# Optimization experiments

Measured on AMD Instinct MI355X. Metric: run time of the kernel, lower is better.

## Reference

```python
import jax, jax.numpy as jnp
import numpy as np
from jax import lax

B, C, H, W = 16, 128, 128, 128
C8, C16 = C // 8, C // 16
LN_EPS = 1e-5


def dct_mat(N):
    # torch_dct.dct (norm=None): X_k = 2 * sum_n x_n cos(pi*(2n+1)k/(2N))
    n = jnp.arange(N, dtype=jnp.float32)
    k = jnp.arange(N, dtype=jnp.float32)
    return 2.0 * jnp.cos(jnp.pi * (2.0 * n[None, :] + 1.0) * k[:, None] / (2.0 * N))


def setup_inputs() -> dict:
    key = jax.random.key(0)
    ks = jax.random.split(key, 20)
    s = 0.05
    return {
        "x": jax.random.normal(ks[0], (B, C, H, W), dtype=jnp.float32),
        # channel attention (1x1 convs acting on GAP -> stored as dense [out,in])
        "ca_w1": jax.random.normal(ks[1], (C8, C), dtype=jnp.float32) * s,
        "ca_b1": jnp.zeros((C8,), jnp.float32),
        "ca_w2": jax.random.normal(ks[2], (C, C8), dtype=jnp.float32) * s,
        "ca_b2": jnp.zeros((C,), jnp.float32),
        # spatial attention 9x9 conv -> 1 channel
        "sa_w": jax.random.normal(ks[3], (1, C, 9, 9), dtype=jnp.float32) * s,
        "sa_b": jnp.zeros((1,), jnp.float32),
        # frequency channel attention MLP
        "fa_w1": jax.random.normal(ks[4], (C8, C), dtype=jnp.float32) * s,
        "fa_b1": jnp.zeros((C8,), jnp.float32),
        "fa_w2": jax.random.normal(ks[5], (C, C8), dtype=jnp.float32) * s,
        "fa_b2": jnp.zeros((C,), jnp.float32),
        # global context block
        "gc_mask_w": jax.random.normal(ks[6], (C,), dtype=jnp.float32) * s,
        "gc_mask_b": jnp.zeros((), jnp.float32),
        "gc_t1_w": jax.random.normal(ks[7], (C16, C), dtype=jnp.float32) * s,
        "gc_t1_b": jnp.zeros((C16,), jnp.float32),
        "gc_ln_g": jnp.ones((C16,), jnp.float32),
        "gc_ln_b": jnp.zeros((C16,), jnp.float32),
        "gc_t2_w": jax.random.normal(ks[8], (C, C16), dtype=jnp.float32) * s,
        "gc_t2_b": jnp.zeros((C,), jnp.float32),
        # branch mixing weights + output 1x1 conv
        "alpha": jnp.ones((4,), jnp.float32),
        "out_w": jax.random.normal(ks[9], (C, C), dtype=jnp.float32) * s,
        "out_b": jnp.zeros((C,), jnp.float32),
    }


def reference(x, ca_w1, ca_b1, ca_w2, ca_b2, sa_w, sa_b,
              fa_w1, fa_b1, fa_w2, fa_b2,
              gc_mask_w, gc_mask_b, gc_t1_w, gc_t1_b, gc_ln_g, gc_ln_b,
              gc_t2_w, gc_t2_b, alpha, out_w, out_b):
    b, c, h, w = x.shape
    # --- channel attention (SE-style) ---
    gap = x.mean(axis=(2, 3))                                   # [B,C]
    hca = jax.nn.relu(gap @ ca_w1.T + ca_b1)
    ca = jax.nn.sigmoid(hca @ ca_w2.T + ca_b2)                  # [B,C]
    ac = x * ca[:, :, None, None]
    # --- spatial attention (9x9 conv -> sigmoid gate) ---
    smap = lax.conv_general_dilated(x, sa_w, (1, 1), ((4, 4), (4, 4)),
                                    dimension_numbers=("NCHW", "OIHW", "NCHW"))
    as_ = jax.nn.sigmoid(smap + sa_b[None, :, None, None]) * x
    # --- frequency channel attention (DCT-II 2d, mean over freq) ---
    Dw = dct_mat(w)
    Dh = dct_mat(h)
    xf = jnp.einsum("bchw,kw->bchk", x, Dw)
    xf = jnp.einsum("bchk,lh->bclk", xf, Dh)                    # [B,C,H,W] freq
    favg = xf.mean(axis=(2, 3))                                 # [B,C]
    hfa = jax.nn.relu(favg @ fa_w1.T + fa_b1)
    fwt = jax.nn.sigmoid(hfa @ fa_w2.T + fa_b2)
    af = x * fwt[:, :, None, None]
    # --- global context block ---
    mask = jnp.einsum("bchw,c->bhw", x, gc_mask_w) + gc_mask_b  # [B,H,W]
    mask = jax.nn.softmax(mask.reshape(b, h * w), axis=-1)      # [B,HW]
    ctx = jnp.einsum("bcp,bp->bc", x.reshape(b, c, h * w), mask)  # [B,C]
    t = ctx @ gc_t1_w.T + gc_t1_b                               # [B,C/16]
    mu = t.mean(axis=-1, keepdims=True)
    var = ((t - mu) ** 2).mean(axis=-1, keepdims=True)
    t = (t - mu) * lax.rsqrt(var + LN_EPS) * gc_ln_g + gc_ln_b
    t = jax.nn.relu(t)
    ctx2 = t @ gc_t2_w.T + gc_t2_b                              # [B,C]
    ag = x + ctx2[:, :, None, None]
    # --- softmax-weighted fusion + output 1x1 conv ---
    wts = jax.nn.softmax(alpha)
    fused = wts[0] * ac + wts[1] * as_ + wts[2] * af + wts[3] * ag
    return jnp.einsum("bchw,oc->bohw", fused, out_w) + out_b[None, :, None, None]
```

## Files before the change

kernel.cpp:

```cpp
#include <hip/hip_runtime.h>
#include <math.h>

#define B_   16
#define C_   128
#define W_   128
#define HW_  16384

#define OFF_SARR 0
#define OFF_GAP  128
#define OFF_FAVG 2176
#define OFF_CTX  4224
#define OFF_G    6272
#define OFF_CB   8320
#define OFF_WTS  10368
#define OFF_PMAX 10496
#define OFF_PSUM 10752
#define OFF_SMX  11008
#define OFF_SINV 11024
#define OFF_M    16384
#define OFF_S    (16384 + 262144)
#define OFF_SMAP (16384 + 2 * 262144)

__device__ __forceinline__ float wave_reduce_sum(float v) {
#pragma unroll
  for (int o = 32; o > 0; o >>= 1) v += __shfl_down(v, o, 64);
  return v;
}

__global__ void k0_sarr(float* __restrict__ sarr) {
  int n = threadIdx.x;
  double a = 3.14159265358979323846 * (2.0 * n + 1.0) / 256.0;
  double v = 2.0 * sin(64.0 * a) * cos(63.5 * a) / sin(0.5 * a);
  sarr[n] = (float)v;
}

__global__ __launch_bounds__(256) void k1_planered(const float* __restrict__ x,
                                                   const float* __restrict__ sarr,
                                                   float* __restrict__ gap,
                                                   float* __restrict__ favg) {
  __shared__ float sL[128];
  __shared__ float buf[8];
  int tid = threadIdx.x;
  int bc = blockIdx.x;
  if (tid < 128) sL[tid] = sarr[tid];
  __syncthreads();
  const float* xp = x + (size_t)bc * HW_;
  float s0 = 0.f, s1 = 0.f;
  for (int i = tid << 2; i < HW_; i += 1024) {
    float4 v = *(const float4*)(xp + i);
    int y = i >> 7, xs = i & 127;
    float shy = sL[y];
    float d = v.x * sL[xs] + v.y * sL[xs + 1] + v.z * sL[xs + 2] + v.w * sL[xs + 3];
    s0 += v.x + v.y + v.z + v.w;
    s1 += shy * d;
  }
  s0 = wave_reduce_sum(s0);
  s1 = wave_reduce_sum(s1);
  int lane = tid & 63, wv = tid >> 6;
  if (lane == 0) { buf[wv] = s0; buf[4 + wv] = s1; }
  __syncthreads();
  if (tid == 0) {
    gap[bc]  = (buf[0] + buf[1] + buf[2] + buf[3]) * (1.f / 16384.f);
    favg[bc] = (buf[4] + buf[5] + buf[6] + buf[7]) * (1.f / 16384.f);
  }
}

__global__ __launch_bounds__(256) void k2_masklogit(const float* __restrict__ x,
                                                    const float* __restrict__ gcw,
                                                    const float* __restrict__ gcb,
                                                    float* __restrict__ m) {
  __shared__ float gl[128];
  int tid = threadIdx.x;
  int b = blockIdx.x >> 4;
  int chunk = blockIdx.x & 15;
  if (tid < 128) gl[tid] = gcw[tid];
  __syncthreads();
  int p0 = (chunk << 10) + (tid << 2);
  const float* xp = x + (size_t)b * C_ * HW_ + p0;
  float4 acc = make_float4(0.f, 0.f, 0.f, 0.f);
  for (int c = 0; c < 128; ++c) {
    float4 v = *(const float4*)(xp + (size_t)c * HW_);
    float wv = gl[c];
    acc.x = fmaf(wv, v.x, acc.x);
    acc.y = fmaf(wv, v.y, acc.y);
    acc.z = fmaf(wv, v.z, acc.z);
    acc.w = fmaf(wv, v.w, acc.w);
  }
  float bb = gcb[0];
  acc.x += bb; acc.y += bb; acc.z += bb; acc.w += bb;
  *(float4*)(m + b * HW_ + p0) = acc;
}

__global__ __launch_bounds__(256) void k3a_part(const float* __restrict__ m,
                                                float* __restrict__ pmax,
                                                float* __restrict__ psum) {
  __shared__ float buf[8];
  int blk = blockIdx.x;
  int tid = threadIdx.x;
  float4 v = *(const float4*)(m + (blk << 10) + (tid << 2));
  float mx = fmaxf(fmaxf(v.x, v.y), fmaxf(v.z, v.w));
#pragma unroll
  for (int o = 32; o > 0; o >>= 1) mx = fmaxf(mx, __shfl_xor(mx, o, 64));
  int lane = tid & 63, wv = tid >> 6;
  if (lane == 0) buf[wv] = mx;
  __syncthreads();
  mx = fmaxf(fmaxf(buf[0], buf[1]), fmaxf(buf[2], buf[3]));
  float s = __expf(v.x - mx) + __expf(v.y - mx) + __expf(v.z - mx) + __expf(v.w - mx);
  s = wave_reduce_sum(s);
  if (lane == 0) buf[4 + wv] = s;
  __syncthreads();
  if (tid == 0) {
    pmax[blk] = mx;
    psum[blk] = buf[4] + buf[5] + buf[6] + buf[7];
  }
}

__global__ void k3b_comb(const float* __restrict__ pmax, const float* __restrict__ psum,
                         float* __restrict__ smx, float* __restrict__ sinv) {
  int tid = threadIdx.x;
  int b = tid >> 4, j = tid & 15;
  float mx = pmax[tid];
  float sm = psum[tid];
  float gmx = mx;
#pragma unroll
  for (int o = 8; o > 0; o >>= 1) gmx = fmaxf(gmx, __shfl_xor(gmx, o, 64));
  float e = sm * __expf(mx - gmx);
#pragma unroll
  for (int o = 8; o > 0; o >>= 1) e += __shfl_xor(e, o, 64);
  if (j == 0) { smx[b] = gmx; sinv[b] = 1.f / e; }
}

__global__ __launch_bounds__(256) void k3c_norm(float* __restrict__ m,
                                                const float* __restrict__ smx,
                                                const float* __restrict__ sinv) {
  int blk = blockIdx.x;
  int b = blk >> 4;
  int i = (blk << 10) + (threadIdx.x << 2);
  float mx = smx[b], inv = sinv[b];
  float4 v = *(const float4*)(m + i);
  v.x = __expf(v.x - mx) * inv;
  v.y = __expf(v.y - mx) * inv;
  v.z = __expf(v.z - mx) * inv;
  v.w = __expf(v.w - mx) * inv;
  *(float4*)(m + i) = v;
}

__global__ __launch_bounds__(256) void k4_ctx(const float* __restrict__ x,
                                              const float* __restrict__ mask,
                                              float* __restrict__ ctx) {
  __shared__ float buf[4];
  int tid = threadIdx.x;
  int bc = blockIdx.x;
  int b = bc >> 7;
  const float* xp = x + (size_t)bc * HW_;
  const float* mp = mask + b * HW_;
  float s = 0.f;
  for (int i = tid << 2; i < HW_; i += 1024) {
    float4 v = *(const float4*)(xp + i);
    float4 mk = *(const float4*)(mp + i);
    s += v.x * mk.x + v.y * mk.y + v.z * mk.z + v.w * mk.w;
  }
  s = wave_reduce_sum(s);
  if ((tid & 63) == 0) buf[tid >> 6] = s;
  __syncthreads();
  if (tid == 0) ctx[bc] = buf[0] + buf[1] + buf[2] + buf[3];
}

__global__ __launch_bounds__(128) void k5_mlp(
    const float* __restrict__ gap, const float* __restrict__ favg,
    const float* __restrict__ ctx,
    const float* __restrict__ ca_w1, const float* __restrict__ ca_b1,
    const float* __restrict__ ca_w2, const float* __restrict__ ca_b2,
    const float* __restrict__ fa_w1, const float* __restrict__ fa_b1,
    const float* __restrict__ fa_w2, const float* __restrict__ fa_b2,
    const float* __restrict__ t1w, const float* __restrict__ t1b,
    const float* __restrict__ lng, const float* __restrict__ lnb,
    const float* __restrict__ t2w, const float* __restrict__ t2b,
    const float* __restrict__ alpha,
    const float* __restrict__ out_w, const float* __restrict__ out_b,
    float* __restrict__ g, float* __restrict__ cb, float* __restrict__ wts) {
  int b = blockIdx.x, t = threadIdx.x;
  __shared__ float gapL[128], favL[128], ctxL[128], hca[16], hfa[16], tl[8], dl[128];
  gapL[t] = gap[(b << 7) + t];
  favL[t] = favg[(b << 7) + t];
  ctxL[t] = ctx[(b << 7) + t];
  __syncthreads();
  if (t < 16) {
    float a = ca_b1[t], f = fa_b1[t];
    for (int c = 0; c < 128; ++c) {
      a += gapL[c] * ca_w1[t * 128 + c];
      f += favL[c] * fa_w1[t * 128 + c];
    }
    hca[t] = fmaxf(a, 0.f);
    hfa[t] = fmaxf(f, 0.f);
  }
  if (t < 8) {
    float v = t1b[t];
    for (int c = 0; c < 128; ++c) v += ctxL[c] * t1w[t * 128 + c];
    tl[t] = v;
  }
  __syncthreads();
  float mu = 0.f;
#pragma unroll
  for (int j = 0; j < 8; ++j) mu += tl[j];
  mu *= 0.125f;
  float var = 0.f;
#pragma unroll
  for (int j = 0; j < 8; ++j) { float d = tl[j] - mu; var += d * d; }
  var *= 0.125f;
  float rs = rsqrtf(var + 1e-5f);
  float a0 = alpha[0], a1 = alpha[1], a2 = alpha[2], a3 = alpha[3];
  float am = fmaxf(fmaxf(a0, a1), fmaxf(a2, a3));
  float e0 = __expf(a0 - am), e1 = __expf(a1 - am), e2 = __expf(a2 - am), e3 = __expf(a3 - am);
  float es = 1.f / (e0 + e1 + e2 + e3);
  float w0 = e0 * es, w1 = e1 * es, w2 = e2 * es, w3 = e3 * es;
  float cav = ca_b2[t], fav = fa_b2[t], c2 = t2b[t];
#pragma unroll
  for (int j = 0; j < 16; ++j) {
    cav += hca[j] * ca_w2[t * 16 + j];
    fav += hfa[j] * fa_w2[t * 16 + j];
  }
#pragma unroll
  for (int j = 0; j < 8; ++j) {
    float tn = fmaxf((tl[j] - mu) * rs * lng[j] + lnb[j], 0.f);
    c2 += tn * t2w[t * 8 + j];
  }
  cav = 1.f / (1.f + __expf(-cav));
  fav = 1.f / (1.f + __expf(-fav));
  g[(b << 7) + t] = w0 * cav + w2 * fav + w3;
  dl[t] = w3 * c2;
  __syncthreads();
  float s = out_b[t];
  for (int c = 0; c < 128; ++c) s += out_w[t * 128 + c] * dl[c];
  cb[(b << 7) + t] = s;
  if (b == 0 && t < 4) wts[t] = (t == 0) ? w0 : (t == 1) ? w1 : (t == 2) ? w2 : w3;
}

template <int CPS>
__global__ __launch_bounds__(256) void k6_conv(const float* __restrict__ x,
                                               const float* __restrict__ saw,
                                               float* __restrict__ smap_part) {
  __shared__ float tile[2][40 * 76];
  int tid = threadIdx.x;
  int t = blockIdx.x;
  int b = blockIdx.y;
  int split = blockIdx.z;
  int y0 = (t >> 1) << 5;
  int x0 = (t & 1) << 6;
  int rg = tid >> 4;
  int cg = tid & 15;
  int r0 = rg << 1;
  int px0 = cg << 2;
  float acc0[4] = {0.f, 0.f, 0.f, 0.f};
  float acc1[4] = {0.f, 0.f, 0.f, 0.f};
  const float* xb = x + (size_t)b * C_ * HW_;
  int c_lo = split * CPS;

  auto stage = [&](int bufi, int c) {
    const float* xc = xb + (size_t)c * HW_;
    float* tb = tile[bufi];
    for (int idx = tid; idx < 720; idx += 256) {
      int row = idx / 18, c4 = idx - row * 18;
      int gy = y0 - 4 + row;
      int gx = x0 - 4 + (c4 << 2);
      float4 v = make_float4(0.f, 0.f, 0.f, 0.f);
      if (gy >= 0 && gy < 128 && gx >= 0 && gx < 128)
        v = *(const float4*)(xc + gy * W_ + gx);
      *(float4*)(tb + row * 76 + (c4 << 2)) = v;
    }
  };

  stage(0, c_lo);
  for (int i = 0; i < CPS; ++i) {
    __syncthreads();
    if (i + 1 < CPS) stage((i + 1) & 1, c_lo + i + 1);
    const float* tb = tile[i & 1];
    const float* wrow = saw + (c_lo + i) * 81;
    float rb[2][12];
    {
      const float* tp = tb + r0 * 76 + px0;
      float4 u0 = *(const float4*)tp, u1 = *(const float4*)(tp + 4), u2 = *(const float4*)(tp + 8);
      rb[0][0] = u0.x; rb[0][1] = u0.y; rb[0][2] = u0.z; rb[0][3] = u0.w;
      rb[0][4] = u1.x; rb[0][5] = u1.y; rb[0][6] = u1.z; rb[0][7] = u1.w;
      rb[0][8] = u2.x; rb[0][9] = u2.y; rb[0][10] = u2.z; rb[0][11] = u2.w;
    }
#pragma unroll
    for (int dy = 0; dy < 9; ++dy) {
      int cur = dy & 1, nxt = cur ^ 1;
      const float* tp = tb + (r0 + dy + 1) * 76 + px0;
      float4 u0 = *(const float4*)tp, u1 = *(const float4*)(tp + 4), u2 = *(const float4*)(tp + 8);
      rb[nxt][0] = u0.x; rb[nxt][1] = u0.y; rb[nxt][2] = u0.z; rb[nxt][3] = u0.w;
      rb[nxt][4] = u1.x; rb[nxt][5] = u1.y; rb[nxt][6] = u1.z; rb[nxt][7] = u1.w;
      rb[nxt][8] = u2.x; rb[nxt][9] = u2.y; rb[nxt][10] = u2.z; rb[nxt][11] = u2.w;
#pragma unroll
      for (int dx = 0; dx < 9; ++dx) {
        float wv = wrow[dy * 9 + dx];
#pragma unroll
        for (int j = 0; j < 4; ++j) {
          acc0[j] = fmaf(wv, rb[cur][dx + j], acc0[j]);
          acc1[j] = fmaf(wv, rb[nxt][dx + j], acc1[j]);
        }
      }
    }
  }
  float* op = smap_part + ((size_t)(split * B_ + b)) * HW_ + (y0 + r0) * W_ + x0 + px0;
  *(float4*)op = make_float4(acc0[0], acc0[1], acc0[2], acc0[3]);
  *(float4*)(op + W_) = make_float4(acc1[0], acc1[1], acc1[2], acc1[3]);
}

template <int NS>
__global__ __launch_bounds__(256) void k6b_gate(const float* __restrict__ smap_part,
                                                const float* __restrict__ wts,
                                                const float* __restrict__ sab,
                                                float* __restrict__ s) {
  int i = (blockIdx.x * 256 + threadIdx.x) << 2;
  float w1 = wts[1];
  float bb = sab[0];
  float4 a = *(const float4*)(smap_part + i);
#pragma unroll
  for (int j = 1; j < NS; ++j) {
    float4 t4 = *(const float4*)(smap_part + (size_t)j * 262144 + i);
    a.x += t4.x; a.y += t4.y; a.z += t4.z; a.w += t4.w;
  }
  float4 r;
  r.x = w1 / (1.f + __expf(-(a.x + bb)));
  r.y = w1 / (1.f + __expf(-(a.y + bb)));
  r.z = w1 / (1.f + __expf(-(a.z + bb)));
  r.w = w1 / (1.f + __expf(-(a.w + bb)));
  *(float4*)(s + i) = r;
}

__global__ __launch_bounds__(256, 2) void k7_gemm(const float* __restrict__ x,
                                                  const float* __restrict__ w,
                                                  const float* __restrict__ g,
                                                  const float* __restrict__ s,
                                                  const float* __restrict__ cb,
                                                  float* __restrict__ out) {
  __shared__ float wT[64 * 128];
  __shared__ float xm[64 * 128];
  int tid = threadIdx.x;
  int b = blockIdx.x >> 7;
  int pt = blockIdx.x & 127;
  int p0 = pt << 7;
  const float* xb = x + (size_t)b * C_ * HW_ + p0;
  const float* sb = s + b * HW_ + p0;
  int pg = tid & 15, og = tid >> 4;
  int o0 = og << 3;
  int ppA = pg << 2;
  int ppB = 64 + (pg << 2);
  float acc[8][8];
#pragma unroll
  for (int i = 0; i < 8; ++i)
#pragma unroll
    for (int j = 0; j < 8; ++j) acc[i][j] = 0.f;
  int sp4 = (tid & 31) << 2;
  float4 sv = *(const float4*)(sb + sp4);
  int crow = tid >> 5;
  int wc4 = tid & 15;
  int wor = tid >> 4;
  for (int chunk = 0; chunk < 2; ++chunk) {
    int cbase = chunk << 6;
    __syncthreads();
#pragma unroll
    for (int pass = 0; pass < 8; ++pass) {
      int c = cbase + (pass << 3) + crow;
      float4 v = *(const float4*)(xb + (size_t)c * HW_ + sp4);
      float gc = g[(b << 7) + c];
      float4 r;
      r.x = v.x * (gc + sv.x);
      r.y = v.y * (gc + sv.y);
      r.z = v.z * (gc + sv.z);
      r.w = v.w * (gc + sv.w);
      *(float4*)(xm + ((c - cbase) << 7) + sp4) = r;
      int o = (pass << 4) + wor;
      float4 wv = *(const float4*)(w + (o << 7) + cbase + (wc4 << 2));
      int qp = (o >> 2) ^ wc4;
      int ob = o & 3;
      int cl = wc4 << 2;
      wT[(cl + 0) * 128 + (qp << 2) + ob] = wv.x;
      wT[(cl + 1) * 128 + (qp << 2) + ob] = wv.y;
      wT[(cl + 2) * 128 + (qp << 2) + ob] = wv.z;
      wT[(cl + 3) * 128 + (qp << 2) + ob] = wv.w;
    }
    __syncthreads();
#pragma unroll 4
    for (int cl = 0; cl < 64; ++cl) {
      int K = cl >> 2;
      const float* wrow = wT + (cl << 7);
      const float* xrow = xm + (cl << 7);
      float4 wa = *(const float4*)(wrow + ((((og << 1)) ^ K) << 2));
      float4 wb = *(const float4*)(wrow + ((((og << 1) | 1) ^ K) << 2));
      float4 xa = *(const float4*)(xrow + ppA);
      float4 xb4 = *(const float4*)(xrow + ppB);
      float wv[8] = {wa.x, wa.y, wa.z, wa.w, wb.x, wb.y, wb.z, wb.w};
      float xv[8] = {xa.x, xa.y, xa.z, xa.w, xb4.x, xb4.y, xb4.z, xb4.w};
#pragma unroll
      for (int i = 0; i < 8; ++i)
#pragma unroll
        for (int j = 0; j < 8; ++j) acc[i][j] = fmaf(wv[i], xv[j], acc[i][j]);
    }
  }
  size_t obase = ((size_t)((b << 7) + o0)) * HW_ + p0;
#pragma unroll
  for (int i = 0; i < 8; ++i) {
    float cv = cb[(b << 7) + o0 + i];
    float4 r0 = make_float4(acc[i][0] + cv, acc[i][1] + cv, acc[i][2] + cv, acc[i][3] + cv);
    float4 r1 = make_float4(acc[i][4] + cv, acc[i][5] + cv, acc[i][6] + cv, acc[i][7] + cv);
    *(float4*)(out + obase + (size_t)i * HW_ + ppA) = r0;
    *(float4*)(out + obase + (size_t)i * HW_ + ppB) = r1;
  }
}

extern "C" void kernel_launch(void* const* d_in, const int* in_sizes, int n_in,
                              void* d_out, int out_size, void* d_ws, size_t ws_size,
                              hipStream_t stream) {
  const float* x       = (const float*)d_in[0];
  const float* ca_w1   = (const float*)d_in[1];
  const float* ca_b1   = (const float*)d_in[2];
  const float* ca_w2   = (const float*)d_in[3];
  const float* ca_b2   = (const float*)d_in[4];
  const float* sa_w    = (const float*)d_in[5];
  const float* sa_b    = (const float*)d_in[6];
  const float* fa_w1   = (const float*)d_in[7];
  const float* fa_b1   = (const float*)d_in[8];
  const float* fa_w2   = (const float*)d_in[9];
  const float* fa_b2   = (const float*)d_in[10];
  const float* gc_mw   = (const float*)d_in[11];
  const float* gc_mb   = (const float*)d_in[12];
  const float* gc_t1w  = (const float*)d_in[13];
  const float* gc_t1b  = (const float*)d_in[14];
  const float* gc_lng  = (const float*)d_in[15];
  const float* gc_lnb  = (const float*)d_in[16];
  const float* gc_t2w  = (const float*)d_in[17];
  const float* gc_t2b  = (const float*)d_in[18];
  const float* alpha   = (const float*)d_in[19];
  const float* out_w   = (const float*)d_in[20];
  const float* out_b   = (const float*)d_in[21];
  float* out = (float*)d_out;
  float* ws = (float*)d_ws;

  float* sarr = ws + OFF_SARR;
  float* gap  = ws + OFF_GAP;
  float* favg = ws + OFF_FAVG;
  float* ctx  = ws + OFF_CTX;
  float* g    = ws + OFF_G;
  float* cb   = ws + OFF_CB;
  float* wts  = ws + OFF_WTS;
  float* pmax = ws + OFF_PMAX;
  float* psum = ws + OFF_PSUM;
  float* smx  = ws + OFF_SMX;
  float* sinv = ws + OFF_SINV;
  float* m    = ws + OFF_M;
  float* s    = ws + OFF_S;
  float* smap = ws + OFF_SMAP;

  size_t need8 = (size_t)(16384 + 10 * 262144) * sizeof(float);
  int use8 = (ws_size >= need8) ? 1 : 0;

  k0_sarr<<<1, 128, 0, stream>>>(sarr);
  k1_planered<<<2048, 256, 0, stream>>>(x, sarr, gap, favg);
  k2_masklogit<<<256, 256, 0, stream>>>(x, gc_mw, gc_mb, m);
  k3a_part<<<256, 256, 0, stream>>>(m, pmax, psum);
  k3b_comb<<<1, 256, 0, stream>>>(pmax, psum, smx, sinv);
  k3c_norm<<<256, 256, 0, stream>>>(m, smx, sinv);
  k4_ctx<<<2048, 256, 0, stream>>>(x, m, ctx);
  k5_mlp<<<16, 128, 0, stream>>>(gap, favg, ctx, ca_w1, ca_b1, ca_w2, ca_b2,
                                 fa_w1, fa_b1, fa_w2, fa_b2, gc_t1w, gc_t1b,
                                 gc_lng, gc_lnb, gc_t2w, gc_t2b, alpha,
                                 out_w, out_b, g, cb, wts);
  if (use8) {
    k6_conv<16><<<dim3(8, 16, 8), 256, 0, stream>>>(x, sa_w, smap);
    k6b_gate<8><<<256, 256, 0, stream>>>(smap, wts, sa_b, s);
  } else {
    k6_conv<32><<<dim3(8, 16, 4), 256, 0, stream>>>(x, sa_w, smap);
    k6b_gate<4><<<256, 256, 0, stream>>>(smap, wts, sa_b, s);
  }
  k7_gemm<<<2048, 256, 0, stream>>>(x, out_w, g, s, cb, out);
}
```

Baseline: 542.7 us.

## Retile 9x9 conv to full-width 4-row tiles and pre-transpose GEMM weights

The spatial conv now stages a full-width 32-row halo tile per channel in one buffer. Each thread computes a 4x4 output patch, so every loaded row is reused across four output rows. The conv also drops the double-buffered prefetch and, when workspace allows, uses 16 channel splits. Separately, a small kernel transposes out_w once into workspace, and the GEMM reads weights straight from global/L2 instead of staging a swizzled copy in LDS. This frees LDS and removes the 2-block occupancy bound, but adds a launch and uncached-in-LDS weight loads in the inner loop.

```diff
diff --git a/kernel.cpp b/kernel.cpp
--- a/kernel.cpp
+++ b/kernel.cpp
@@ -17,9 +17,10 @@
 #define OFF_PSUM 10752
 #define OFF_SMX  11008
 #define OFF_SINV 11024
-#define OFF_M    16384
-#define OFF_S    (16384 + 262144)
-#define OFF_SMAP (16384 + 2 * 262144)
+#define OFF_WT   16384
+#define OFF_M    32768
+#define OFF_S    (32768 + 262144)
+#define OFF_SMAP (32768 + 2 * 262144)
 
 __device__ __forceinline__ float wave_reduce_sum(float v) {
 #pragma unroll
@@ -240,72 +241,65 @@
 __global__ __launch_bounds__(256) void k6_conv(const float* __restrict__ x,
                                                const float* __restrict__ saw,
                                                float* __restrict__ smap_part) {
-  __shared__ float tile[2][40 * 76];
-  int tid = threadIdx.x;
-  int t = blockIdx.x;
+  __shared__ float tile[40 * 136];
+  int tid = threadIdx.x;
+  int yt = blockIdx.x;
   int b = blockIdx.y;
   int split = blockIdx.z;
-  int y0 = (t >> 1) << 5;
-  int x0 = (t & 1) << 6;
-  int rg = tid >> 4;
-  int cg = tid & 15;
-  int r0 = rg << 1;
+  int y0 = yt << 5;
+  int rg = tid >> 5;
+  int cg = tid & 31;
+  int r0 = rg << 2;
   int px0 = cg << 2;
-  float acc0[4] = {0.f, 0.f, 0.f, 0.f};
-  float acc1[4] = {0.f, 0.f, 0.f, 0.f};
+  float acc[4][4];
+#pragma unroll
+  for (int i = 0; i < 4; ++i)
+#pragma unroll
+    for (int j = 0; j < 4; ++j) acc[i][j] = 0.f;
   const float* xb = x + (size_t)b * C_ * HW_;
   int c_lo = split * CPS;
 
-  auto stage = [&](int bufi, int c) {
+  for (int ci = 0; ci < CPS; ++ci) {
+    int c = c_lo + ci;
     const float* xc = xb + (size_t)c * HW_;
-    float* tb = tile[bufi];
-    for (int idx = tid; idx < 720; idx += 256) {
-      int row = idx / 18, c4 = idx - row * 18;
+    __syncthreads();
+    for (int idx = tid; idx < 1360; idx += 256) {
+      int row = idx / 34, c4 = idx - row * 34;
       int gy = y0 - 4 + row;
-      int gx = x0 - 4 + (c4 << 2);
+      int gx = (c4 << 2) - 4;
       float4 v = make_float4(0.f, 0.f, 0.f, 0.f);
-      if (gy >= 0 && gy < 128 && gx >= 0 && gx < 128)
+      if (gy >= 0 && gy < 128 && gx >= 0 && gx <= 124)
         v = *(const float4*)(xc + gy * W_ + gx);
-      *(float4*)(tb + row * 76 + (c4 << 2)) = v;
+      *(float4*)(tile + row * 136 + (c4 << 2)) = v;
     }
-  };
-
-  stage(0, c_lo);
-  for (int i = 0; i < CPS; ++i) {
     __syncthreads();
-    if (i + 1 < CPS) stage((i + 1) & 1, c_lo + i + 1);
-    const float* tb = tile[i & 1];
-    const float* wrow = saw + (c_lo + i) * 81;
-    float rb[2][12];
-    {
-      const float* tp = tb + r0 * 76 + px0;
-      float4 u0 = *(const float4*)tp, u1 = *(const float4*)(tp + 4), u2 = *(const float4*)(tp + 8);
-      rb[0][0] = u0.x; rb[0][1] = u0.y; rb[0][2] = u0.z; rb[0][3] = u0.w;
-      rb[0][4] = u1.x; rb[0][5] = u1.y; rb[0][6] = u1.z; rb[0][7] = u1.w;
-      rb[0][8] = u2.x; rb[0][9] = u2.y; rb[0][10] = u2.z; rb[0][11] = u2.w;
-    }
-#pragma unroll
-    for (int dy = 0; dy < 9; ++dy) {
-      int cur = dy & 1, nxt = cur ^ 1;
-      const float* tp = tb + (r0 + dy + 1) * 76 + px0;
-      float4 u0 = *(const float4*)tp, u1 = *(const float4*)(tp + 4), u2 = *(const float4*)(tp + 8);
-      rb[nxt][0] = u0.x; rb[nxt][1] = u0.y; rb[nxt][2] = u0.z; rb[nxt][3] = u0.w;
-      rb[nxt][4] = u1.x; rb[nxt][5] = u1.y; rb[nxt][6] = u1.z; rb[nxt][7] = u1.w;
-      rb[nxt][8] = u2.x; rb[nxt][9] = u2.y; rb[nxt][10] = u2.z; rb[nxt][11] = u2.w;
-#pragma unroll
-      for (int dx = 0; dx < 9; ++dx) {
-        float wv = wrow[dy * 9 + dx];
-#pragma unroll
-        for (int j = 0; j < 4; ++j) {
-          acc0[j] = fmaf(wv, rb[cur][dx + j], acc0[j]);
-          acc1[j] = fmaf(wv, rb[nxt][dx + j], acc1[j]);
+    const float* wrow = saw + c * 81;
+#pragma unroll
+    for (int ir = 0; ir < 12; ++ir) {
+      const float* tp = tile + (r0 + ir) * 136 + px0;
+      float4 u0 = *(const float4*)tp;
+      float4 u1 = *(const float4*)(tp + 4);
+      float4 u2 = *(const float4*)(tp + 8);
+      float rowv[12] = {u0.x, u0.y, u0.z, u0.w, u1.x, u1.y, u1.z, u1.w,
+                        u2.x, u2.y, u2.z, u2.w};
+#pragma unroll
+      for (int i = 0; i < 4; ++i) {
+        int dy = ir - i;
+        if (dy < 0 || dy > 8) continue;
+#pragma unroll
+        for (int dx = 0; dx < 9; ++dx) {
+          float wv = wrow[dy * 9 + dx];
+#pragma unroll
+          for (int j = 0; j < 4; ++j)
+            acc[i][j] = fmaf(wv, rowv[dx + j], acc[i][j]);
         }
       }
     }
   }
-  float* op = smap_part + ((size_t)(split * B_ + b)) * HW_ + (y0 + r0) * W_ + x0 + px0;
-  *(float4*)op = make_float4(acc0[0], acc0[1], acc0[2], acc0[3]);
-  *(float4*)(op + W_) = make_float4(acc1[0], acc1[1], acc1[2], acc1[3]);
+  float* op = smap_part + ((size_t)(split * B_ + b)) * HW_ + (y0 + r0) * W_ + px0;
+#pragma unroll
+  for (int i = 0; i < 4; ++i)
+    *(float4*)(op + (size_t)i * W_) = make_float4(acc[i][0], acc[i][1], acc[i][2], acc[i][3]);
 }
 
 template <int NS>
@@ -330,13 +324,26 @@
   *(float4*)(s + i) = r;
 }
 
-__global__ __launch_bounds__(256, 2) void k7_gemm(const float* __restrict__ x,
-                                                  const float* __restrict__ w,
-                                                  const float* __restrict__ g,
-                                                  const float* __restrict__ s,
-                                                  const float* __restrict__ cb,
-                                                  float* __restrict__ out) {
-  __shared__ float wT[64 * 128];
+__global__ __launch_bounds__(256) void k7a_transpose(const float* __restrict__ w,
+                                                     float* __restrict__ wt) {
+  __shared__ float t[32][33];
+  int bx = blockIdx.x & 3, by = blockIdx.x >> 2;
+  int lx = threadIdx.x & 31, ly = threadIdx.x >> 5;
+#pragma unroll
+  for (int j = 0; j < 4; ++j)
+    t[ly + j * 8][lx] = w[(by * 32 + ly + j * 8) * 128 + bx * 32 + lx];
+  __syncthreads();
+#pragma unroll
+  for (int j = 0; j < 4; ++j)
+    wt[(bx * 32 + ly + j * 8) * 128 + by * 32 + lx] = t[lx][ly + j * 8];
+}
+
+__global__ __launch_bounds__(256) void k7_gemm(const float* __restrict__ x,
+                                               const float* __restrict__ wt,
+                                               const float* __restrict__ g,
+                                               const float* __restrict__ s,
+                                               const float* __restrict__ cb,
+                                               float* __restrict__ out) {
   __shared__ float xm[64 * 128];
   int tid = threadIdx.x;
   int b = blockIdx.x >> 7;
@@ -354,16 +361,15 @@
 #pragma unroll
     for (int j = 0; j < 8; ++j) acc[i][j] = 0.f;
   int sp4 = (tid & 31) << 2;
+  int crow = tid >> 5;
   float4 sv = *(const float4*)(sb + sp4);
-  int crow = tid >> 5;
-  int wc4 = tid & 15;
-  int wor = tid >> 4;
   for (int chunk = 0; chunk < 2; ++chunk) {
     int cbase = chunk << 6;
     __syncthreads();
 #pragma unroll
     for (int pass = 0; pass < 8; ++pass) {
-      int c = cbase + (pass << 3) + crow;
+      int cl = (pass << 3) + crow;
+      int c = cbase + cl;
       float4 v = *(const float4*)(xb + (size_t)c * HW_ + sp4);
       float gc = g[(b << 7) + c];
       float4 r;
@@ -371,25 +377,15 @@
       r.y = v.y * (gc + sv.y);
       r.z = v.z * (gc + sv.z);
       r.w = v.w * (gc + sv.w);
-      *(float4*)(xm + ((c - cbase) << 7) + sp4) = r;
-      int o = (pass << 4) + wor;
-      float4 wv = *(const float4*)(w + (o << 7) + cbase + (wc4 << 2));
-      int qp = (o >> 2) ^ wc4;
-      int ob = o & 3;
-      int cl = wc4 << 2;
-      wT[(cl + 0) * 128 + (qp << 2) + ob] = wv.x;
-      wT[(cl + 1) * 128 + (qp << 2) + ob] = wv.y;
-      wT[(cl + 2) * 128 + (qp << 2) + ob] = wv.z;
-      wT[(cl + 3) * 128 + (qp << 2) + ob] = wv.w;
+      *(float4*)(xm + (cl << 7) + sp4) = r;
     }
     __syncthreads();
 #pragma unroll 4
     for (int cl = 0; cl < 64; ++cl) {
-      int K = cl >> 2;
-      const float* wrow = wT + (cl << 7);
+      const float* wp = wt + ((size_t)(cbase + cl) << 7) + o0;
+      float4 wa = *(const float4*)wp;
+      float4 wb = *(const float4*)(wp + 4);
       const float* xrow = xm + (cl << 7);
-      float4 wa = *(const float4*)(wrow + ((((og << 1)) ^ K) << 2));
-      float4 wb = *(const float4*)(wrow + ((((og << 1) | 1) ^ K) << 2));
       float4 xa = *(const float4*)(xrow + ppA);
       float4 xb4 = *(const float4*)(xrow + ppB);
       float wv[8] = {wa.x, wa.y, wa.z, wa.w, wb.x, wb.y, wb.z, wb.w};
@@ -450,12 +446,13 @@
   float* psum = ws + OFF_PSUM;
   float* smx  = ws + OFF_SMX;
   float* sinv = ws + OFF_SINV;
+  float* wt   = ws + OFF_WT;
   float* m    = ws + OFF_M;
   float* s    = ws + OFF_S;
   float* smap = ws + OFF_SMAP;
 
-  size_t need8 = (size_t)(16384 + 10 * 262144) * sizeof(float);
-  int use8 = (ws_size >= need8) ? 1 : 0;
+  size_t need16 = (size_t)(OFF_SMAP + 16 * 262144) * sizeof(float);
+  size_t need8  = (size_t)(OFF_SMAP + 8 * 262144) * sizeof(float);
 
   k0_sarr<<<1, 128, 0, stream>>>(sarr);
   k1_planered<<<2048, 256, 0, stream>>>(x, sarr, gap, favg);
@@ -468,12 +465,16 @@
                                  fa_w1, fa_b1, fa_w2, fa_b2, gc_t1w, gc_t1b,
                                  gc_lng, gc_lnb, gc_t2w, gc_t2b, alpha,
                                  out_w, out_b, g, cb, wts);
-  if (use8) {
-    k6_conv<16><<<dim3(8, 16, 8), 256, 0, stream>>>(x, sa_w, smap);
+  k7a_transpose<<<16, 256, 0, stream>>>(out_w, wt);
+  if (ws_size >= need16) {
+    k6_conv<8><<<dim3(4, 16, 16), 256, 0, stream>>>(x, sa_w, smap);
+    k6b_gate<16><<<256, 256, 0, stream>>>(smap, wts, sa_b, s);
+  } else if (ws_size >= need8) {
+    k6_conv<16><<<dim3(4, 16, 8), 256, 0, stream>>>(x, sa_w, smap);
     k6b_gate<8><<<256, 256, 0, stream>>>(smap, wts, sa_b, s);
   } else {
-    k6_conv<32><<<dim3(8, 16, 4), 256, 0, stream>>>(x, sa_w, smap);
+    k6_conv<32><<<dim3(4, 16, 4), 256, 0, stream>>>(x, sa_w, smap);
     k6b_gate<4><<<256, 256, 0, stream>>>(smap, wts, sa_b, s);
   }
-  k7_gemm<<<2048, 256, 0, stream>>>(x, out_w, g, s, cb, out);
-}
+  k7_gemm<<<2048, 256, 0, stream>>>(x, wt, g, s, cb, out);
+}
```

New measurement: 532.1 us. About the same (-2.0%).
